# Performance work log

Measured on AMD Instinct MI355X. Metric: run time of the kernel, lower is better.

Reference implementation:

```python
import jax, jax.numpy as jnp
import numpy as np

HEADS = 16
DIM_HEAD = 64

def setup_inputs() -> dict:
    key = jax.random.key(0)
    k1, k2, k3 = jax.random.split(key, 3)
    B, F, N, DIM = 4, 16, 196, 1024
    ntok = 1 + F * N  # cls + frames*patches
    x = jax.random.normal(k1, (B, ntok, DIM), dtype=jnp.float32)
    w_qkv = jax.random.normal(k2, (DIM, 3 * HEADS * DIM_HEAD), dtype=jnp.float32) * (DIM ** -0.5)
    w_out = jax.random.normal(k3, (HEADS * DIM_HEAD, DIM), dtype=jnp.float32) * ((HEADS * DIM_HEAD) ** -0.5)
    return {"x": x, "w_qkv": w_qkv, "w_out": w_out, "f": F}

def _attn(q, k, v):
    # q: [b, i, d], k/v: [b, j, d]
    sim = jnp.einsum('bid,bjd->bij', q, k)
    a = jax.nn.softmax(sim, axis=-1)
    return jnp.einsum('bij,bjd->bid', a, v)

def reference(x, w_qkv, w_out, f):
    B, ntok, dim = x.shape
    h, dh = HEADS, DIM_HEAD
    n = (ntok - 1) // f  # patches per frame
    scale = dh ** -0.5

    qkv = x @ w_qkv  # [B, ntok, 3*h*dh]
    q, k, v = jnp.split(qkv, 3, axis=-1)
    # 'b n (h d) -> (b h) n d'
    def split_heads(t):
        return t.reshape(B, ntok, h, dh).transpose(0, 2, 1, 3).reshape(B * h, ntok, dh)
    q, k, v = split_heads(q) * scale, split_heads(k), split_heads(v)

    cls_q, q_ = q[:, :1], q[:, 1:]
    cls_k, k_ = k[:, :1], k[:, 1:]
    cls_v, v_ = v[:, :1], v[:, 1:]

    # cls token attends to everything
    cls_out = _attn(cls_q, k, v)  # [(b h), 1, d]

    # axial rearrange: '(b h) (f n) d -> (b h f) n d' (spatial attention)
    def to_axial(t):
        return t.reshape(B * h, f, n, dh).reshape(B * h * f, n, dh)
    q_, k_, v_ = map(to_axial, (q_, k_, v_))

    # broadcast cls kv to each frame: 'b () d -> (b r) () d', r = f
    cls_k_r = jnp.repeat(cls_k, f, axis=0)
    cls_v_r = jnp.repeat(cls_v, f, axis=0)
    k_ = jnp.concatenate((cls_k_r, k_), axis=1)  # [(b h f), 1+n, d]
    v_ = jnp.concatenate((cls_v_r, v_), axis=1)

    out = _attn(q_, k_, v_)  # [(b h f), n, d]
    # back: '(b h f) n d -> (b h) (f n) d'
    out = out.reshape(B * h, f * n, dh)
    out = jnp.concatenate((cls_out, out), axis=1)  # [(b h), ntok, d]
    # '(b h) n d -> b n (h d)'
    out = out.reshape(B, h, ntok, dh).transpose(0, 2, 1, 3).reshape(B, ntok, h * dh)
    return out @ w_out
```

## Files before the change

kernel.cpp:

```cpp
#include <hip/hip_runtime.h>
#include <stdint.h>

typedef unsigned short u16;
typedef unsigned int u32;
typedef __attribute__((ext_vector_type(4))) float f32x4;
typedef __attribute__((ext_vector_type(4))) float float4v;
typedef __attribute__((ext_vector_type(8))) short short8;
typedef __attribute__((ext_vector_type(4))) u32 u32x4;
typedef __attribute__((ext_vector_type(4))) u16 u16x4;
typedef __attribute__((ext_vector_type(8))) u16 u16x8;

#define DEV static __device__ __forceinline__

#define NTOK 3137
#define MROWS 12548
#define NHEAD 16
#define DH 64
#define NKS 32

DEV float bf2f(u16 h){ u32 u = ((u32)h)<<16; float f; __builtin_memcpy(&f,&u,4); return f; }
DEV u16 f2bf(float f){ u32 u; __builtin_memcpy(&u,&f,4); u32 r = u + 0x7FFFu + ((u>>16)&1u); return (u16)(r>>16); }

DEV void gl_lds16(const u16* g, u16* l){
  __builtin_amdgcn_global_load_lds((const __attribute__((address_space(1))) void*)g,
                                   (__attribute__((address_space(3))) void*)l, 16, 0, 0);
}

#define BARRIER()  asm volatile("s_barrier" ::: "memory")
#define WAIT_LGKM0() asm volatile("s_waitcnt lgkmcnt(0)" ::: "memory")
#define WAIT_VM(n)  asm volatile("s_waitcnt vmcnt(" #n ")" ::: "memory")

__global__ __launch_bounds__(256) void prep_kernel(
    const float* __restrict__ x, const float* __restrict__ wqkv, const float* __restrict__ wout,
    u16* __restrict__ xb, u16* __restrict__ wqkvT, u16* __restrict__ woutT)
{
  __shared__ float tile[32][33];
  const int bid = blockIdx.x, tid = threadIdx.x;
  if(bid < 2048){
    const int n4 = (MROWS*1024)/4;
    for(int i = bid*256 + tid; i < n4; i += 2048*256){
      float4v v = *(const float4v*)(x + (size_t)i*4);
      u16x4 o;
      for(int e=0;e<4;++e) o[e] = f2bf(v[e]);
      *(u16x4*)(xb + (size_t)i*4) = o;
    }
  } else {
    const float* in; u16* out; int C, c0, r0;
    if(bid < 2048+3072){
      int tb = bid - 2048; in = wqkv; out = wqkvT; C = 3072;
      c0 = (tb%96)<<5; r0 = (tb/96)<<5;
    } else {
      int tb = bid - 5120; in = wout; out = woutT; C = 1024;
      c0 = (tb&31)<<5; r0 = (tb>>5)<<5;
    }
    const int R = 1024;
    int tx = tid&31, ty = tid>>5;
    for(int k=0;k<32;k+=8) tile[ty+k][tx] = in[(size_t)(r0+ty+k)*C + c0+tx];
    __syncthreads();
    for(int k=0;k<32;k+=8) out[(size_t)(c0+ty+k)*R + r0+tx] = f2bf(tile[tx][ty+k]);
  }
}

template<int EPI>
__global__ __launch_bounds__(256, 2) void gemm_kernel(
    const u16* __restrict__ A, const u16* __restrict__ Bt,
    u16* __restrict__ Qb, u16* __restrict__ Kb, u16* __restrict__ Vb,
    float* __restrict__ Out, int Mtot, int tilesx)
{
  __shared__ __align__(16) char smem[73728];
  const int tid = threadIdx.x, lane = tid & 63, wid = tid >> 6;
  const int wc = wid;

  const int nwg = gridDim.x, orig = blockIdx.x;
  const int q = nwg >> 3, r = nwg & 7;
  const int xcd = orig & 7, sidx = orig >> 3;
  const int wg = (xcd < r ? xcd*(q+1) : r*(q+1) + (xcd-r)*q) + sidx;
  const int by = wg / tilesx, bx = wg - by*tilesx;
  const int m0 = by << 7, n0 = bx << 8;

  f32x4 acc[8][4];
  #pragma unroll
  for(int i=0;i<8;++i)
    #pragma unroll
    for(int j=0;j<4;++j) acc[i][j] = (f32x4){0.f,0.f,0.f,0.f};

  auto STAGE = [&](int t){
    char* rbase = smem + (t%3)*24576;
    #pragma unroll
    for(int c=0;c<6;++c){
      const int isB = (c >= 2);
      int slotpos = (isB ? (c-2)<<8 : (c<<8)) + tid;
      int pair = slotpos >> 3;
      int sl   = (slotpos & 7) ^ (pair & 7);
      int grow = (isB ? n0 : m0) + pair*2 + (sl>>2);
      if(!isB && grow >= Mtot) grow = Mtot - 1;
      const u16* src = (isB ? Bt : A) + (size_t)grow*1024 + t*32 + (sl&3)*8;
      u16* dst = (u16*)(rbase + (isB ? 8192 + ((c-2)<<12) : (c<<12)) + wid*1024);
      gl_lds16(src, dst);
    }
  };

  const int pl = (lane&15)>>1;
  const int sprime = ((((lane&1)<<2) | (lane>>4)) ^ pl);
  const int laneoff = pl*128 + sprime*16;

  auto PHASE = [&](int t){
    const char* rb = smem + (t%3)*24576;
    short8 af[8], bfv[4];
    #pragma unroll
    for(int i=0;i<8;++i) af[i]  = *(const short8*)(rb + (i<<10) + laneoff);
    #pragma unroll
    for(int j=0;j<4;++j) bfv[j] = *(const short8*)(rb + 8192 + (wc<<12) + (j<<10) + laneoff);
    const bool st = (t+2 < NKS);
    if(st) STAGE(t+2);
    BARRIER();
    WAIT_LGKM0();
    __builtin_amdgcn_s_setprio(1);
    #pragma unroll
    for(int i=0;i<8;++i)
      #pragma unroll
      for(int j=0;j<4;++j)
        acc[i][j] = __builtin_amdgcn_mfma_f32_16x16x32_bf16(af[i], bfv[j], acc[i][j], 0,0,0);
    __builtin_amdgcn_s_setprio(0);
    if(st){ WAIT_VM(6); } else { WAIT_VM(0); }
    BARRIER();
  };

  STAGE(0); STAGE(1);
  WAIT_VM(6);
  BARRIER();

  for(int t=0; t<NKS; ++t) PHASE(t);

  __syncthreads();

  if constexpr(EPI==0){
    const int which = n0 >> 10;
    const int hbase = (n0 & 1023) >> 6;
    const float sc = (which==0) ? 0.125f : 1.0f;
    u16* dst = (which==0)?Qb:((which==1)?Kb:Vb);
    u16* lC = (u16*)smem;
    #pragma unroll
    for(int i=0;i<8;++i){
      int rr = (i<<4) + ((lane>>4)<<2);
      #pragma unroll
      for(int j=0;j<4;++j){
        int ct = (wc<<6) + (j<<4) + (lane&15);
        #pragma unroll
        for(int rg=0;rg<4;++rg) lC[(rr+rg)*264 + ct] = f2bf(acc[i][j][rg]*sc);
      }
    }
    __syncthreads();
    for(int it=0; it<16; ++it){
      int idx = it*256 + tid;
      int row = idx >> 5, rest = idx & 31, hh = rest>>3, slot = rest&7;
      int mm = m0 + row;
      if(mm < Mtot){
        int b = mm / NTOK, tok = mm - b*NTOK;
        u16x8 v = *(const u16x8*)&lC[row*264 + hh*64 + slot*8];
        *(u16x8*)(dst + (((size_t)(b*NHEAD + hbase + hh)*NTOK + tok)<<6) + slot*8) = v;
      }
    }
  } else {
    #pragma unroll
    for(int i=0;i<8;++i){
      #pragma unroll
      for(int j=0;j<4;++j){
        int gc = n0 + (wc<<6) + (j<<4) + (lane&15);
        #pragma unroll
        for(int rg=0;rg<4;++rg){
          int gr = m0 + (i<<4) + ((lane>>4)<<2) + rg;
          if(gr < Mtot) Out[(size_t)gr*1024 + gc] = acc[i][j][rg];
        }
      }
    }
  }
}

__global__ __launch_bounds__(256) void attn_kernel(
    const u16* __restrict__ Qb, const u16* __restrict__ Kb, const u16* __restrict__ Vb,
    float* __restrict__ part, u16* __restrict__ Abuf)
{
  __shared__ u16 lV[64*232];
  __shared__ u16 lP[4*16*232];
  __shared__ float qs[64];
  __shared__ float pbuf[4][64];
  __shared__ float wmx[4], wls[4];
  __shared__ float wacc[4][64];
  const int tid = threadIdx.x, lane = tid & 63, wv = tid >> 6;

  if(blockIdx.x >= 1024){
    const int idx = blockIdx.x - 1024;
    const int c = idx >> 6, bh = idx & 63;
    const u16* Kh = Kb + (size_t)bh*NTOK*DH;
    const u16* Vh = Vb + (size_t)bh*NTOK*DH;
    if(tid < 64) qs[tid] = bf2f(Qb[(size_t)bh*NTOK*DH + tid]);
    __syncthreads();

    const int jb = c*256 + wv*64;
    const int j = jb + lane;
    float s = -1e30f;
    if(j < NTOK){
      const u16* kr = Kh + (size_t)j*DH;
      float dot = 0.f;
      for(int t=0;t<8;++t){
        u16x8 kv = *(const u16x8*)(kr + t*8);
        for(int e=0;e<8;++e) dot += bf2f(kv[e]) * qs[t*8+e];
      }
      s = dot;
    }
    float mw = s;
    for(int off=1; off<64; off<<=1) mw = fmaxf(mw, __shfl_xor(mw, off));
    float p = (j < NTOK) ? __expf(s - mw) : 0.f;
    float lw = p;
    for(int off=1; off<64; off<<=1) lw += __shfl_xor(lw, off);
    pbuf[wv][lane] = p;

    float accd = 0.f;
    if(jb < NTOK){
      int nv = NTOK - jb; if(nv > 64) nv = 64;
      for(int jj=0; jj<nv; ++jj)
        accd += pbuf[wv][jj] * bf2f(Vh[(size_t)(jb+jj)*DH + lane]);
    }
    wacc[wv][lane] = accd;
    if(lane==0){ wmx[wv]=mw; wls[wv]=lw; }
    __syncthreads();
    if(wv==0){
      float M = fmaxf(fmaxf(wmx[0],wmx[1]), fmaxf(wmx[2],wmx[3]));
      float L=0.f, Acc=0.f;
      for(int wi=0; wi<4; ++wi){
        float e = __expf(wmx[wi]-M);
        L += wls[wi]*e; Acc += wacc[wi][lane]*e;
      }
      float* dstp = part + ((size_t)bh*13 + c)*68;
      if(lane==0){ dstp[0]=M; dstp[1]=L; }
      dstp[2+lane] = Acc;
    }
    return;
  }

  const int bf = blockIdx.x, bh = bf >> 4, fi = bf & 15;
  const u16* Kh = Kb + (size_t)bh*NTOK*DH;
  const u16* Vh = Vb + (size_t)bh*NTOK*DH;
  const u16* Qh = Qb + (size_t)bh*NTOK*DH;

  for(int c = tid; c < 224*8; c += 256){
    int tok = c >> 3, slot = c & 7;
    u16 vals[8];
    if(tok <= 196){
      size_t row = (tok==0) ? 0 : (size_t)(fi*196 + tok)*DH;
      u16x8 v = *(const u16x8*)(Vh + row + slot*8);
      for(int e=0;e<8;++e) vals[e] = v[e];
    } else {
      for(int e=0;e<8;++e) vals[e] = 0;
    }
    for(int e=0;e<8;++e) lV[(slot*8+e)*232 + tok] = vals[e];
  }
  for(int c = tid; c < 4*16*16; c += 256){
    int w2 = c >> 8, rem = c & 255, row = rem >> 4, cc = rem & 15;
    lP[w2*(16*232) + row*232 + 208 + cc] = 0;
  }
  __syncthreads();

  u16* myP = lP + wv*(16*232);
  const int b_i = bh >> 4, h = bh & 15;

  for(int qt = wv; qt < 13; qt += 4){
    int qr = qt*16 + (lane&15);
    int qrc = qr < 196 ? qr : 195;
    size_t qrow = (size_t)(1 + fi*196 + qrc)*DH;
    short8 qa0 = *(const short8*)(Qh + qrow + ((lane>>4)<<3));
    short8 qa1 = *(const short8*)(Qh + qrow + 32 + ((lane>>4)<<3));

    f32x4 s[13];
    for(int t=0;t<13;++t){
      int tok = t*16 + (lane&15);
      int tokc = tok < 197 ? tok : 196;
      size_t krow = (tokc==0) ? 0 : (size_t)(fi*196 + tokc)*DH;
      short8 b0v = *(const short8*)(Kh + krow + ((lane>>4)<<3));
      short8 b1v = *(const short8*)(Kh + krow + 32 + ((lane>>4)<<3));
      f32x4 z = {0.f,0.f,0.f,0.f};
      z = __builtin_amdgcn_mfma_f32_16x16x32_bf16(qa0, b0v, z, 0,0,0);
      z = __builtin_amdgcn_mfma_f32_16x16x32_bf16(qa1, b1v, z, 0,0,0);
      s[t] = z;
    }
    int mycol = lane & 15;
    if(192 + mycol >= 197)
      for(int r=0;r<4;++r) s[12][r] = -1e30f;

    f32x4 mx = s[0];
    for(int t=1;t<13;++t) for(int r=0;r<4;++r) mx[r] = fmaxf(mx[r], s[t][r]);
    for(int off=1; off<16; off<<=1)
      for(int r=0;r<4;++r) mx[r] = fmaxf(mx[r], __shfl_xor(mx[r], off));
    f32x4 lsum = {0.f,0.f,0.f,0.f};
    for(int t=0;t<13;++t) for(int r=0;r<4;++r){
      float p = __expf(s[t][r] - mx[r]); s[t][r] = p; lsum[r] += p;
    }
    for(int off=1; off<16; off<<=1)
      for(int r=0;r<4;++r) lsum[r] += __shfl_xor(lsum[r], off);

    for(int t=0;t<13;++t){
      int tok = t*16 + mycol;
      for(int r=0;r<4;++r) myP[(((lane>>4)<<2)+r)*232 + tok] = f2bf(s[t][r]);
    }

    f32x4 o[4] = {{0.f,0.f,0.f,0.f},{0.f,0.f,0.f,0.f},{0.f,0.f,0.f,0.f},{0.f,0.f,0.f,0.f}};
    for(int t2=0;t2<7;++t2){
      short8 a = *(const short8*)&myP[(lane&15)*232 + t2*32 + ((lane>>4)<<3)];
      for(int nd=0;nd<4;++nd){
        short8 b = *(const short8*)&lV[(nd*16 + (lane&15))*232 + t2*32 + ((lane>>4)<<3)];
        o[nd] = __builtin_amdgcn_mfma_f32_16x16x32_bf16(a, b, o[nd], 0,0,0);
      }
    }

    for(int nd=0; nd<4; ++nd){
      int d = nd*16 + (lane&15);
      for(int r=0;r<4;++r){
        int rr = ((lane>>4)<<2) + r;
        myP[rr*72 + d] = f2bf(o[nd][r] / lsum[r]);
      }
    }
    asm volatile("s_waitcnt lgkmcnt(0)" ::: "memory");
    for(int it=0; it<2; ++it){
      int idx = it*64 + lane;
      int row = idx >> 3, slot = idx & 7;
      int ql = qt*16 + row;
      if(ql < 196){
        u16x8 v = *(const u16x8*)&myP[row*72 + slot*8];
        int tok = 1 + fi*196 + ql;
        *(u16x8*)(Abuf + ((size_t)b_i*NTOK + tok)*1024 + h*DH + slot*8) = v;
      }
    }
  }
}

__global__ __launch_bounds__(64) void cls_reduce_kernel(
    const float* __restrict__ part, u16* __restrict__ Abuf)
{
  const int lane = threadIdx.x, bh = blockIdx.x;
  const float* p0 = part + (size_t)bh*13*68;
  float M = -1e30f;
  for(int i=0;i<13;++i) M = fmaxf(M, p0[i*68]);
  float L=0.f, Acc=0.f;
  for(int i=0;i<13;++i){
    float e = __expf(p0[i*68] - M);
    L += p0[i*68+1]*e;
    Acc += p0[i*68+2+lane]*e;
  }
  int b = bh>>4, h = bh&15;
  Abuf[(size_t)b*NTOK*1024 + h*DH + lane] = f2bf(Acc/L);
}

extern "C" void kernel_launch(void* const* d_in, const int* in_sizes, int n_in,
                              void* d_out, int out_size, void* d_ws, size_t ws_size,
                              hipStream_t stream) {
  const float* x     = (const float*)d_in[0];
  const float* wqkv  = (const float*)d_in[1];
  const float* wout  = (const float*)d_in[2];
  float* out = (float*)d_out;
  char* ws = (char*)d_ws;

  u16* xb     = (u16*)(ws);
  u16* Abuf   = xb;
  u16* wqkvT  = (u16*)(ws + 25698304);
  float* clsPart = (float*)(ws + 25698304);
  u16* woutT  = (u16*)(ws + 31989760);
  u16* Qb     = (u16*)(ws + 34086912);
  u16* Kb     = (u16*)(ws + 59785216);
  u16* Vb     = (u16*)(ws + 85483520);

  prep_kernel<<<dim3(6144), dim3(256), 0, stream>>>(x, wqkv, wout, xb, wqkvT, woutT);

  gemm_kernel<0><<<dim3(1188), dim3(256), 0, stream>>>(xb, wqkvT, Qb, Kb, Vb, nullptr, MROWS, 12);

  attn_kernel<<<dim3(1856), dim3(256), 0, stream>>>(Qb, Kb, Vb, clsPart, Abuf);
  cls_reduce_kernel<<<dim3(64), dim3(64), 0, stream>>>(clsPart, Abuf);

  gemm_kernel<1><<<dim3(396), dim3(256), 0, stream>>>(Abuf, woutT, nullptr, nullptr, nullptr, out, MROWS, 4);
}
```

Before: 197.5 us.

## Enlarge GEMM tiles to 256x256 with 8 waves and 4-stage register double-buffered pipeline

The GEMM kernels now use 512-thread blocks with a 2x4 wave grid, computing 256x256 output tiles instead of 128x256. This raises operand reuse per LDS load and halves the grid size. The k-loop moves to a 4-deep LDS ring that prefetches three stages ahead, with fragment reads double-buffered in registers so the next step's LDS reads overlap the current MFMAs. It uses 128KB LDS, which limits occupancy to one block per CU, and the epilogue is split into two halves to reuse LDS. The 600- and 200-block grids may leave CUs idle in the last wave.

```diff
diff --git a/kernel.cpp b/kernel.cpp
--- a/kernel.cpp
+++ b/kernel.cpp
@@ -27,7 +27,6 @@
 }
 
 #define BARRIER()  asm volatile("s_barrier" ::: "memory")
-#define WAIT_LGKM0() asm volatile("s_waitcnt lgkmcnt(0)" ::: "memory")
 #define WAIT_VM(n)  asm volatile("s_waitcnt vmcnt(" #n ")" ::: "memory")
 
 __global__ __launch_bounds__(256) void prep_kernel(
@@ -62,21 +61,21 @@
 }
 
 template<int EPI>
-__global__ __launch_bounds__(256, 2) void gemm_kernel(
+__global__ __launch_bounds__(512, 2) void gemm_kernel(
     const u16* __restrict__ A, const u16* __restrict__ Bt,
     u16* __restrict__ Qb, u16* __restrict__ Kb, u16* __restrict__ Vb,
     float* __restrict__ Out, int Mtot, int tilesx)
 {
-  __shared__ __align__(16) char smem[73728];
+  __shared__ __align__(16) char smem[131072];
   const int tid = threadIdx.x, lane = tid & 63, wid = tid >> 6;
-  const int wc = wid;
+  const int wr = wid >> 2, wc = wid & 3;
 
   const int nwg = gridDim.x, orig = blockIdx.x;
   const int q = nwg >> 3, r = nwg & 7;
   const int xcd = orig & 7, sidx = orig >> 3;
   const int wg = (xcd < r ? xcd*(q+1) : r*(q+1) + (xcd-r)*q) + sidx;
   const int by = wg / tilesx, bx = wg - by*tilesx;
-  const int m0 = by << 7, n0 = bx << 8;
+  const int m0 = by << 8, n0 = bx << 8;
 
   f32x4 acc[8][4];
   #pragma unroll
@@ -85,17 +84,18 @@
     for(int j=0;j<4;++j) acc[i][j] = (f32x4){0.f,0.f,0.f,0.f};
 
   auto STAGE = [&](int t){
-    char* rbase = smem + (t%3)*24576;
-    #pragma unroll
-    for(int c=0;c<6;++c){
-      const int isB = (c >= 2);
-      int slotpos = (isB ? (c-2)<<8 : (c<<8)) + tid;
+    char* rbase = smem + (t&3)*32768;
+    #pragma unroll
+    for(int c=0;c<4;++c){
+      const int half = c & 1;
+      const int isB  = c >> 1;
+      int slotpos = (half<<9) + tid;
       int pair = slotpos >> 3;
       int sl   = (slotpos & 7) ^ (pair & 7);
       int grow = (isB ? n0 : m0) + pair*2 + (sl>>2);
       if(!isB && grow >= Mtot) grow = Mtot - 1;
       const u16* src = (isB ? Bt : A) + (size_t)grow*1024 + t*32 + (sl&3)*8;
-      u16* dst = (u16*)(rbase + (isB ? 8192 + ((c-2)<<12) : (c<<12)) + wid*1024);
+      u16* dst = (u16*)(rbase + (isB<<14) + (half<<13) + wid*1024);
       gl_lds16(src, dst);
     }
   };
@@ -104,33 +104,44 @@
   const int sprime = ((((lane&1)<<2) | (lane>>4)) ^ pl);
   const int laneoff = pl*128 + sprime*16;
 
-  auto PHASE = [&](int t){
-    const char* rb = smem + (t%3)*24576;
-    short8 af[8], bfv[4];
-    #pragma unroll
-    for(int i=0;i<8;++i) af[i]  = *(const short8*)(rb + (i<<10) + laneoff);
-    #pragma unroll
-    for(int j=0;j<4;++j) bfv[j] = *(const short8*)(rb + 8192 + (wc<<12) + (j<<10) + laneoff);
-    const bool st = (t+2 < NKS);
-    if(st) STAGE(t+2);
-    BARRIER();
-    WAIT_LGKM0();
+  auto RDFRAGS = [&](int t, short8 (&f)[12]){
+    const char* rb = smem + (t&3)*32768;
+    #pragma unroll
+    for(int i=0;i<8;++i) f[i]   = *(const short8*)(rb + (wr<<13) + (i<<10) + laneoff);
+    #pragma unroll
+    for(int j=0;j<4;++j) f[8+j] = *(const short8*)(rb + 16384 + (wc<<12) + (j<<10) + laneoff);
+  };
+
+  auto MFMAS = [&](short8 (&f)[12]){
     __builtin_amdgcn_s_setprio(1);
     #pragma unroll
     for(int i=0;i<8;++i)
       #pragma unroll
       for(int j=0;j<4;++j)
-        acc[i][j] = __builtin_amdgcn_mfma_f32_16x16x32_bf16(af[i], bfv[j], acc[i][j], 0,0,0);
+        acc[i][j] = __builtin_amdgcn_mfma_f32_16x16x32_bf16(f[i], f[8+j], acc[i][j], 0,0,0);
     __builtin_amdgcn_s_setprio(0);
-    if(st){ WAIT_VM(6); } else { WAIT_VM(0); }
+  };
+
+  short8 fA[12], fB[12];
+
+  STAGE(0); STAGE(1); STAGE(2);
+  WAIT_VM(4);
+  BARRIER();
+  RDFRAGS(0, fA);
+
+  for(int u=0; u<NKS/2; ++u){
+    const int t0 = 2*u, t1 = 2*u+1;
+    RDFRAGS(t0+1, fB);
+    if(t0+3 < NKS) STAGE(t0+3);
+    MFMAS(fA);
+    if(t0 <= NKS-3){ WAIT_VM(4); } else { WAIT_VM(0); }
     BARRIER();
-  };
-
-  STAGE(0); STAGE(1);
-  WAIT_VM(6);
-  BARRIER();
-
-  for(int t=0; t<NKS; ++t) PHASE(t);
+    if(t1+1 < NKS) RDFRAGS(t1+1, fA);
+    if(t1+3 < NKS) STAGE(t1+3);
+    MFMAS(fB);
+    if(t1 <= NKS-3){ WAIT_VM(4); } else { WAIT_VM(0); }
+    BARRIER();
+  }
 
   __syncthreads();
 
@@ -140,26 +151,31 @@
     const float sc = (which==0) ? 0.125f : 1.0f;
     u16* dst = (which==0)?Qb:((which==1)?Kb:Vb);
     u16* lC = (u16*)smem;
-    #pragma unroll
-    for(int i=0;i<8;++i){
-      int rr = (i<<4) + ((lane>>4)<<2);
-      #pragma unroll
-      for(int j=0;j<4;++j){
-        int ct = (wc<<6) + (j<<4) + (lane&15);
+    for(int rh=0; rh<2; ++rh){
+      if(wr == rh){
         #pragma unroll
-        for(int rg=0;rg<4;++rg) lC[(rr+rg)*264 + ct] = f2bf(acc[i][j][rg]*sc);
-      }
-    }
-    __syncthreads();
-    for(int it=0; it<16; ++it){
-      int idx = it*256 + tid;
-      int row = idx >> 5, rest = idx & 31, hh = rest>>3, slot = rest&7;
-      int mm = m0 + row;
-      if(mm < Mtot){
-        int b = mm / NTOK, tok = mm - b*NTOK;
-        u16x8 v = *(const u16x8*)&lC[row*264 + hh*64 + slot*8];
-        *(u16x8*)(dst + (((size_t)(b*NHEAD + hbase + hh)*NTOK + tok)<<6) + slot*8) = v;
-      }
+        for(int i=0;i<8;++i){
+          int rr = (i<<4) + ((lane>>4)<<2);
+          #pragma unroll
+          for(int j=0;j<4;++j){
+            int ct = (wc<<6) + (j<<4) + (lane&15);
+            #pragma unroll
+            for(int rg=0;rg<4;++rg) lC[(rr+rg)*264 + ct] = f2bf(acc[i][j][rg]*sc);
+          }
+        }
+      }
+      __syncthreads();
+      for(int it=0; it<8; ++it){
+        int idx = it*512 + tid;
+        int row = idx >> 5, rest = idx & 31, hh = rest>>3, slot = rest&7;
+        int mm = m0 + rh*128 + row;
+        if(mm < Mtot){
+          int b = mm / NTOK, tok = mm - b*NTOK;
+          u16x8 v = *(const u16x8*)&lC[row*264 + hh*64 + slot*8];
+          *(u16x8*)(dst + (((size_t)(b*NHEAD + hbase + hh)*NTOK + tok)<<6) + slot*8) = v;
+        }
+      }
+      __syncthreads();
     }
   } else {
     #pragma unroll
@@ -169,7 +185,7 @@
         int gc = n0 + (wc<<6) + (j<<4) + (lane&15);
         #pragma unroll
         for(int rg=0;rg<4;++rg){
-          int gr = m0 + (i<<4) + ((lane>>4)<<2) + rg;
+          int gr = m0 + (wr<<7) + (i<<4) + ((lane>>4)<<2) + rg;
           if(gr < Mtot) Out[(size_t)gr*1024 + gc] = acc[i][j][rg];
         }
       }
@@ -371,10 +387,10 @@
 
   prep_kernel<<<dim3(6144), dim3(256), 0, stream>>>(x, wqkv, wout, xb, wqkvT, woutT);
 
-  gemm_kernel<0><<<dim3(1188), dim3(256), 0, stream>>>(xb, wqkvT, Qb, Kb, Vb, nullptr, MROWS, 12);
+  gemm_kernel<0><<<dim3(600), dim3(512), 0, stream>>>(xb, wqkvT, Qb, Kb, Vb, nullptr, MROWS, 12);
 
   attn_kernel<<<dim3(1856), dim3(256), 0, stream>>>(Qb, Kb, Vb, clsPart, Abuf);
   cls_reduce_kernel<<<dim3(64), dim3(64), 0, stream>>>(clsPart, Abuf);
 
-  gemm_kernel<1><<<dim3(396), dim3(256), 0, stream>>>(Abuf, woutT, nullptr, nullptr, nullptr, out, MROWS, 4);
-}
+  gemm_kernel<1><<<dim3(200), dim3(512), 0, stream>>>(Abuf, woutT, nullptr, nullptr, nullptr, out, MROWS, 4);
+}
```

Measured after the change: 205.7 us. 4.1% more time.
